# Optimization experiments

Hardware: AMD Instinct MI355X
Metric: run time of the kernel (lower is better)

Reference implementation:

```python
import jax, jax.numpy as jnp
import numpy as np
from jax import lax

G, K, KS = 4, 16, 3            # stripes, latents per stripe, support kernel
TEMP, TOPK_RATIO, GATE, EPS = 0.125, 0.125, 0.05, 1e-6


def _l2norm(v):
    # F.normalize(p=2, dim=-1): divide by max(norm, 1e-12)
    return v / jnp.maximum(jnp.linalg.norm(v, axis=-1, keepdims=True), 1e-12)


def _avg_pool3(x):
    # 3x3 avg pool, stride 1, pad 1, count_include_pad=True (torch default)
    s = lax.reduce_window(x, 0.0, lax.add, (1, 1, KS, KS), (1, 1, 1, 1),
                          [(0, 0), (0, 0), (KS // 2, KS // 2), (KS // 2, KS // 2)])
    return s / float(KS * KS)


def setup_inputs() -> dict:
    key = jax.random.key(0)
    k1, k2 = jax.random.split(key)
    x = jax.random.normal(k1, (64, 256, 64, 44), dtype=jnp.float32)
    latent_basis = jax.random.normal(k2, (G, K, 256), dtype=jnp.float32) * 0.05
    return {"x": x, "latent_basis": latent_basis}


def reference(x, latent_basis):
    n, c, h, w = x.shape
    hs = h // G
    # 'n c (g hs) w -> (n g) c hs w'
    sf = x.reshape(n, c, G, hs, w).transpose(0, 2, 1, 3, 4).reshape(n * G, c, hs, w)
    support_feat = _avg_pool3(sf)
    feat_flat = sf.reshape(n, G, c, hs * w).transpose(0, 1, 3, 2)          # n g p c
    supp_flat = support_feat.reshape(n, G, c, hs * w).transpose(0, 1, 3, 2)  # n g p c
    # active mask from detached energy
    e = jnp.mean(lax.stop_gradient(sf) ** 2, axis=1)                       # [n*G, hs, w]
    e = e / jnp.maximum(jnp.max(e, axis=(-2, -1), keepdims=True), EPS)
    am = (e > GATE).astype(jnp.float32)
    fb = (e > 0).astype(jnp.float32)
    use_fb = jnp.sum(am, axis=(-2, -1), keepdims=True) <= 0
    am = jnp.where(use_fb, fb, am).reshape(n, G, hs * w)                   # n g p
    # routing
    sfn = _l2norm(supp_flat)
    lb = _l2norm(latent_basis)                                             # g k c
    logits = jnp.einsum('ngpc,gkc->ngpk', sfn, lb) / TEMP
    route = jax.nn.softmax(logits, axis=-1)
    supp = route * am[..., None]                                           # n g p k
    pw = supp / jnp.maximum(jnp.sum(supp, axis=2, keepdims=True), EPS)
    tokens = jnp.einsum('ngpk,ngpc->ngkc', pw, feat_flat)                  # n g k c
    tokens = tokens.transpose(0, 3, 1, 2).reshape(n, c, G * K)             # n c (g k)
    # presence via top-k over positions
    p = supp.shape[2]
    topk = max(1, min(p, int(p * TOPK_RATIO)))
    vals = lax.top_k(supp.transpose(0, 1, 3, 2), topk)[0]                  # n g k topk
    pres = jnp.mean(vals, axis=-1).reshape(n, G * K)
    pres = pres / jnp.maximum(jnp.sum(pres, axis=1, keepdims=True), EPS)
    return tokens, pres
```

## Files before the change

### kernel.cpp

```cpp
#include <hip/hip_runtime.h>
#include <cstdint>


#define C_ 256
#define W_ 44
#define P_ 704
#define CH_STRIDE 2816
#define NB_STRIDE 720896
#define TOPK_ 88
#define GATE_ 0.05f
#define EPS_ 1e-6f

__global__ __launch_bounds__(256) void k_norm_basis(const float* __restrict__ lb,
                                                    float* __restrict__ lbn) {
  int gk = blockIdx.x;
  int t = threadIdx.x;
  float v = lb[gk * 256 + t];
  float ss = v * v;
  #pragma unroll
  for (int off = 32; off >= 1; off >>= 1) ss += __shfl_xor(ss, off);
  __shared__ float red[4];
  if ((t & 63) == 0) red[t >> 6] = ss;
  __syncthreads();
  float tot = red[0] + red[1] + red[2] + red[3];
  float scale = 1.f / fmaxf(sqrtf(tot), 1e-12f);
  int g = gk >> 4, k = gk & 15;
  lbn[((g * 256 + t) << 4) + k] = v * scale;
}

__global__ __launch_bounds__(1024) void k_route(const float* __restrict__ x,
                                                const float* __restrict__ lbn,
                                                float* __restrict__ supp_kp,
                                                float* __restrict__ supp_pk,
                                                float* __restrict__ invden_ws) {
  __shared__ float lbn_l[4096];
  __shared__ float rsl[11264];
  __shared__ float redA[16];
  __shared__ float redB[16];
  __shared__ float redM[2];
  __shared__ float red2[16 * 16];

  const int tid = threadIdx.x;
  const int w = tid >> 6;
  const int l = tid & 63;
  const bool act = (l < 44);
  const int s = blockIdx.x, n = s >> 2, g = s & 3;
  const int p = w * 44 + l;

  for (int i = tid; i < 4096; i += 1024) lbn_l[i] = lbn[(g << 12) + i];

  const int lsafe = act ? l : 0;
  const float* xb = x + (size_t)n * NB_STRIDE + (g * 16 + w) * 44 + lsafe;
  const float* xm = xb + ((w > 0)  ? -44 : 0);
  const float* xp = xb + ((w < 15) ?  44 : 0);
  const bool hm = (w > 0), hp = (w < 15);

  float rawdot[16];
  #pragma unroll
  for (int k = 0; k < 16; k++) rawdot[k] = 0.f;
  float sq = 0.f, pw2 = 0.f;

  __syncthreads();

  for (int c = 0; c < 256; c += 4) {
    float vm[4], v0[4], vp[4];
    #pragma unroll
    for (int j = 0; j < 4; j++) {
      const size_t o = (size_t)(c + j) * CH_STRIDE;
      vm[j] = xm[o]; v0[j] = xb[o]; vp[j] = xp[o];
    }
    #pragma unroll
    for (int j = 0; j < 4; j++) {
      float a  = act ? v0[j] : 0.f;
      float am_ = (act && hm) ? vm[j] : 0.f;
      float ap_ = (act && hp) ? vp[j] : 0.f;
      float vs = am_ + a + ap_;
      float lf = __shfl(vs, (l + 63) & 63);
      float rt = __shfl(vs, (l + 1) & 63);
      float win = lf + vs + rt;
      pw2 = fmaf(win, win, pw2);
      sq  = fmaf(a, a, sq);
      const float4* wp = (const float4*)&lbn_l[(c + j) << 4];
      float4 w0 = wp[0], w1 = wp[1], w2 = wp[2], w3 = wp[3];
      rawdot[0]  = fmaf(a, w0.x, rawdot[0]);  rawdot[1]  = fmaf(a, w0.y, rawdot[1]);
      rawdot[2]  = fmaf(a, w0.z, rawdot[2]);  rawdot[3]  = fmaf(a, w0.w, rawdot[3]);
      rawdot[4]  = fmaf(a, w1.x, rawdot[4]);  rawdot[5]  = fmaf(a, w1.y, rawdot[5]);
      rawdot[6]  = fmaf(a, w1.z, rawdot[6]);  rawdot[7]  = fmaf(a, w1.w, rawdot[7]);
      rawdot[8]  = fmaf(a, w2.x, rawdot[8]);  rawdot[9]  = fmaf(a, w2.y, rawdot[9]);
      rawdot[10] = fmaf(a, w2.z, rawdot[10]); rawdot[11] = fmaf(a, w2.w, rawdot[11]);
      rawdot[12] = fmaf(a, w3.x, rawdot[12]); rawdot[13] = fmaf(a, w3.y, rawdot[13]);
      rawdot[14] = fmaf(a, w3.z, rawdot[14]); rawdot[15] = fmaf(a, w3.w, rawdot[15]);
    }
  }

  float e_raw = sq * (1.f / 256.f);
  float m = e_raw;
  #pragma unroll
  for (int off = 32; off >= 1; off >>= 1) m = fmaxf(m, __shfl_xor(m, off));
  if (l == 0) redA[w] = m;
  __syncthreads();
  if (tid == 0) {
    float mm = redA[0];
    for (int w2 = 1; w2 < 16; w2++) mm = fmaxf(mm, redA[w2]);
    redM[0] = mm;
  }
  __syncthreads();
  float M = fmaxf(redM[0], EPS_);
  float e = e_raw / M;
  float am = (e > GATE_) ? 1.f : 0.f;
  float fb = (e_raw > 0.f) ? 1.f : 0.f;
  float a = am;
  #pragma unroll
  for (int off = 32; off >= 1; off >>= 1) a += __shfl_xor(a, off);
  if (l == 0) redB[w] = a;
  __syncthreads();
  if (tid == 0) {
    float sm = 0.f;
    for (int w2 = 0; w2 < 16; w2++) sm += redB[w2];
    redM[1] = sm;
  }
  __syncthreads();
  if (redM[1] <= 0.f) am = fb;

  if (act) {
    #pragma unroll
    for (int k = 0; k < 16; k++) rsl[k * 704 + p] = rawdot[k];
  }
  __syncthreads();

  float pd[16];
  #pragma unroll
  for (int k = 0; k < 16; k++) pd[k] = 0.f;
  if (act) {
    #pragma unroll
    for (int dy = -1; dy <= 1; dy++) {
      int yy = w + dy;
      if (yy < 0 || yy > 15) continue;
      #pragma unroll
      for (int dx = -1; dx <= 1; dx++) {
        int xx = l + dx;
        if (xx < 0 || xx > 43) continue;
        int pp = yy * 44 + xx;
        #pragma unroll
        for (int k = 0; k < 16; k++) pd[k] += rsl[k * 704 + pp];
      }
    }
  }

  float pnorm = sqrtf(pw2) * (1.f / 9.f);
  float invn = 1.f / fmaxf(pnorm, 1e-12f);
  float scl = invn * (8.f / 9.f);
  float li[16];
  float mx = -1e30f;
  #pragma unroll
  for (int k = 0; k < 16; k++) { li[k] = pd[k] * scl; mx = fmaxf(mx, li[k]); }
  float ssum = 0.f;
  #pragma unroll
  for (int k = 0; k < 16; k++) { li[k] = __expf(li[k] - mx); ssum += li[k]; }
  float rs2 = am / ssum;
  float supp[16];
  #pragma unroll
  for (int k = 0; k < 16; k++) supp[k] = li[k] * rs2;

  if (act) {
    float* sbp = supp_kp + (size_t)s * (16 * 704);
    #pragma unroll
    for (int k = 0; k < 16; k++) sbp[k * 704 + p] = supp[k];
    float* spk = supp_pk + ((size_t)s * 704 + p) * 16;
    #pragma unroll
    for (int kq = 0; kq < 4; kq++)
      ((float4*)spk)[kq] = make_float4(supp[kq*4+0], supp[kq*4+1],
                                       supp[kq*4+2], supp[kq*4+3]);
  }

  #pragma unroll
  for (int k = 0; k < 16; k++) {
    float v2 = act ? supp[k] : 0.f;
    #pragma unroll
    for (int off = 32; off >= 1; off >>= 1) v2 += __shfl_xor(v2, off);
    if (l == 0) red2[w * 16 + k] = v2;
  }
  __syncthreads();
  if (tid < 16) {
    float den = 0.f;
    for (int w2 = 0; w2 < 16; w2++) den += red2[w2 * 16 + tid];
    invden_ws[s * 16 + tid] = 1.f / fmaxf(den, EPS_);
  }
}

__global__ __launch_bounds__(256) void k_topk(const float* __restrict__ supp_kp,
                                              float* __restrict__ presraw) {
  const int blk = blockIdx.x;
  const int t = threadIdx.x;
  const int lane = t & 63, w = t >> 6;
  const float* v = supp_kp + (size_t)blk * 704;
  const bool h2 = (t < 192);
  uint32_t key0 = __float_as_uint(v[t]);
  uint32_t key1 = __float_as_uint(v[t + 256]);
  uint32_t key2 = h2 ? __float_as_uint(v[t + 512]) : 0u;

  __shared__ uint32_t hist[256];
  __shared__ uint32_t sarr[257];
  __shared__ uint32_t wsum[4];
  __shared__ uint32_t bc0, bc1;
  uint32_t prefix = 0, remaining = TOPK_;

  for (int b = 3; b >= 0; b--) {
    hist[t] = 0u;
    __syncthreads();
    const int shift = b * 8;
    uint32_t mhi = (b == 3) ? 0u : (0xFFFFFFFFu << (shift + 8));
    if ((key0 & mhi) == (prefix & mhi)) atomicAdd(&hist[(key0 >> shift) & 255u], 1u);
    if ((key1 & mhi) == (prefix & mhi)) atomicAdd(&hist[(key1 >> shift) & 255u], 1u);
    if (h2 && ((key2 & mhi) == (prefix & mhi))) atomicAdd(&hist[(key2 >> shift) & 255u], 1u);
    __syncthreads();

    uint32_t val = hist[t];
    #pragma unroll
    for (int off = 1; off < 64; off <<= 1) {
      uint32_t o = (uint32_t)__shfl_down((int)val, off);
      if (lane + off < 64) val += o;
    }
    if (lane == 0) wsum[w] = val;
    __syncthreads();
    uint32_t add = 0;
    for (int w2 = w + 1; w2 < 4; w2++) add += wsum[w2];
    sarr[t] = val + add;
    if (t == 0) sarr[256] = 0u;
    __syncthreads();
    uint32_t s_t = sarr[t], s_n = sarr[t + 1];
    if (s_t >= remaining && s_n < remaining) {
      bc0 = prefix | ((uint32_t)t << shift);
      bc1 = remaining - s_n;
    }
    __syncthreads();
    prefix = bc0; remaining = bc1;
    __syncthreads();
  }

  float tf = __uint_as_float(prefix);
  float sgt = 0.f;
  uint32_t cgt = 0;
  if (key0 > prefix) { sgt += __uint_as_float(key0); cgt++; }
  if (key1 > prefix) { sgt += __uint_as_float(key1); cgt++; }
  if (h2 && key2 > prefix) { sgt += __uint_as_float(key2); cgt++; }
  #pragma unroll
  for (int off = 32; off >= 1; off >>= 1) {
    sgt += __shfl_xor(sgt, off);
    cgt += __shfl_xor(cgt, off);
  }
  __shared__ float rsx[4];
  __shared__ uint32_t rcx[4];
  if (lane == 0) { rsx[w] = sgt; rcx[w] = cgt; }
  __syncthreads();
  if (t == 0) {
    float stot = rsx[0] + rsx[1] + rsx[2] + rsx[3];
    uint32_t ctot = rcx[0] + rcx[1] + rcx[2] + rcx[3];
    float top = stot + (float)(TOPK_ - ctot) * tf;
    presraw[blk] = top * (1.f / (float)TOPK_);
  }
}

__global__ __launch_bounds__(512, 4) void k_tokens(const float* __restrict__ x,
                                                   const float* __restrict__ supp_pk,
                                                   const float* __restrict__ invden,
                                                   float* __restrict__ out) {
  __shared__ float xl[4096];
  const int tid = threadIdx.x;
  const int bid = blockIdx.x;
  const int s = bid >> 1, chalf = bid & 1;
  const int n = s >> 2, g = s & 3;
  const int cl = tid & 127;
  const int q = tid >> 7;
  const int sblk = s * (704 * 16);

  const float* xs = x + (size_t)n * NB_STRIDE + (size_t)(chalf * 128) * CH_STRIDE + g * P_;

  const int li0 = tid, li1 = tid + 512;
  const int lc0 = li0 >> 3, lj0 = li0 & 7;
  const int lc1 = li1 >> 3, lj1 = li1 & 7;
  const float* gp0 = xs + (size_t)lc0 * CH_STRIDE + lj0 * 4;
  const float* gp1 = xs + (size_t)lc1 * CH_STRIDE + lj1 * 4;
  const int wo0 = lc0 * 32 + ((lj0 * 4) ^ ((lc0 & 7) * 4));
  const int wo1 = lc1 * 32 + ((lj1 * 4) ^ ((lc1 & 7) * 4));

  const int sw = (cl & 7) * 4;
  const int rbase = cl * 32;

  float acc[16];
  #pragma unroll
  for (int k = 0; k < 16; k++) acc[k] = 0.f;

  float4 r0 = *(const float4*)gp0;
  float4 r1 = *(const float4*)gp1;
  *(float4*)&xl[wo0] = r0;
  *(float4*)&xl[wo1] = r1;
  __syncthreads();

  for (int tt = 0; tt < 22; tt++) {
    const int p0 = tt * 32;
    float4 n0, n1;
    if (tt < 21) {
      n0 = *(const float4*)(gp0 + p0 + 32);
      n1 = *(const float4*)(gp1 + p0 + 32);
    }

    #pragma unroll
    for (int jj = 0; jj < 8; jj += 4) {
      const int pp0 = q * 8 + jj;
      float4 xv = *(const float4*)&xl[rbase + (pp0 ^ sw)];
      float xa[4] = {xv.x, xv.y, xv.z, xv.w};
      #pragma unroll
      for (int dj = 0; dj < 4; dj++) {
        int uofs = __builtin_amdgcn_readfirstlane(sblk + (p0 + pp0 + dj) * 16);
        const float4* sp = (const float4*)(supp_pk + uofs);
        float4 s0 = sp[0], s1 = sp[1], s2 = sp[2], s3 = sp[3];
        float a = xa[dj];
        acc[0]  += a * s0.x; acc[1]  += a * s0.y; acc[2]  += a * s0.z; acc[3]  += a * s0.w;
        acc[4]  += a * s1.x; acc[5]  += a * s1.y; acc[6]  += a * s1.z; acc[7]  += a * s1.w;
        acc[8]  += a * s2.x; acc[9]  += a * s2.y; acc[10] += a * s2.z; acc[11] += a * s2.w;
        acc[12] += a * s3.x; acc[13] += a * s3.y; acc[14] += a * s3.z; acc[15] += a * s3.w;
      }
    }

    __syncthreads();
    if (tt < 21) {
      *(float4*)&xl[wo0] = n0;
      *(float4*)&xl[wo1] = n1;
      __syncthreads();
    }
  }

  if (q >= 2) {
    float* dst = &xl[((q - 2) * 128 + cl) * 16];
    #pragma unroll
    for (int kq = 0; kq < 4; kq++)
      ((float4*)dst)[kq] = make_float4(acc[kq*4], acc[kq*4+1], acc[kq*4+2], acc[kq*4+3]);
  }
  __syncthreads();
  if (q < 2) {
    const float* src = &xl[(q * 128 + cl) * 16];
    #pragma unroll
    for (int k = 0; k < 16; k++) acc[k] += src[k];
  }
  __syncthreads();
  if (q == 1) {
    float* dst = &xl[cl * 16];
    #pragma unroll
    for (int kq = 0; kq < 4; kq++)
      ((float4*)dst)[kq] = make_float4(acc[kq*4], acc[kq*4+1], acc[kq*4+2], acc[kq*4+3]);
  }
  __syncthreads();
  if (q == 0) {
    const float* src = &xl[cl * 16];
    float* op = out + ((size_t)(n * 256 + chalf * 128 + cl) * 64) + g * 16;
    #pragma unroll
    for (int kq = 0; kq < 4; kq++) {
      int u = __builtin_amdgcn_readfirstlane(s * 16 + kq * 4);
      const float4 iv = *(const float4*)(invden + u);
      float4 o;
      o.x = (acc[kq*4+0] + src[kq*4+0]) * iv.x;
      o.y = (acc[kq*4+1] + src[kq*4+1]) * iv.y;
      o.z = (acc[kq*4+2] + src[kq*4+2]) * iv.z;
      o.w = (acc[kq*4+3] + src[kq*4+3]) * iv.w;
      ((float4*)op)[kq] = o;
    }
  }
}

__global__ __launch_bounds__(64) void k_pres(const float* __restrict__ presraw,
                                             float* __restrict__ out) {
  const int n = blockIdx.x, t = threadIdx.x;
  float v = presraw[n * 64 + t];
  float ssum = v;
  #pragma unroll
  for (int off = 32; off >= 1; off >>= 1) ssum += __shfl_xor(ssum, off);
  out[1048576 + n * 64 + t] = v / fmaxf(ssum, EPS_);
}

extern "C" void kernel_launch(void* const* d_in, const int* in_sizes, int n_in,
                              void* d_out, int out_size, void* d_ws, size_t ws_size,
                              hipStream_t stream) {
  (void)in_sizes; (void)n_in; (void)out_size; (void)ws_size;
  const float* x  = (const float*)d_in[0];
  const float* lb = (const float*)d_in[1];
  float* out = (float*)d_out;
  float* ws = (float*)d_ws;
  float* lbn_ws     = ws;
  float* invden_ws  = ws + 16384;
  float* presraw_ws = ws + 20480;
  float* supp_kp_ws = ws + 24576;
  float* supp_pk_ws = ws + 2908160;

  k_norm_basis<<<64, 256, 0, stream>>>(lb, lbn_ws);
  k_route<<<256, 1024, 0, stream>>>(x, lbn_ws, supp_kp_ws, supp_pk_ws, invden_ws);
  k_topk<<<4096, 256, 0, stream>>>(supp_kp_ws, presraw_ws);
  k_tokens<<<512, 512, 0, stream>>>(x, supp_pk_ws, invden_ws, out);
  k_pres<<<64, 64, 0, stream>>>(presraw_ws, out);
}
```

Before: 358.9 us.

## Split routing kernel over channel halves with partial-sum finalize kernel

The routing kernel previously ran one 1024-thread block per stripe (256 blocks), which leaves many compute units idle on a large GPU. It is now split into a partial kernel over two channel halves (512 blocks) that writes per-position dot products, energy and pooled-norm partials to workspace, plus a finalize kernel that sums them and runs the shared epilogue. This adds an extra launch and a round trip of the partials through global memory, and the old path is kept as a fallback when the workspace is too small. The tokens kernel's launch bounds are also raised to 8 blocks per CU, which may force fewer registers per thread.

```diff
diff --git a/kernel.cpp b/kernel.cpp
--- a/kernel.cpp
+++ b/kernel.cpp
@@ -10,6 +10,7 @@
 #define TOPK_ 88
 #define GATE_ 0.05f
 #define EPS_ 1e-6f
+#define PSLAB 12672
 
 __global__ __launch_bounds__(256) void k_norm_basis(const float* __restrict__ lb,
                                                     float* __restrict__ lbn) {
@@ -26,6 +27,109 @@
   float scale = 1.f / fmaxf(sqrtf(tot), 1e-12f);
   int g = gk >> 4, k = gk & 15;
   lbn[((g * 256 + t) << 4) + k] = v * scale;
+}
+
+__device__ __forceinline__ void route_epilogue(
+    int s, int w, int l, bool act, int p,
+    float* rawdot, float sq, float pw2,
+    float* rsl, float* redA, float* redB, float* redM, float* red2,
+    float* __restrict__ supp_kp, float* __restrict__ supp_pk,
+    float* __restrict__ invden_ws) {
+  const int tid = w * 64 + l;
+  float e_raw = sq * (1.f / 256.f);
+  float m = e_raw;
+  #pragma unroll
+  for (int off = 32; off >= 1; off >>= 1) m = fmaxf(m, __shfl_xor(m, off));
+  if (l == 0) redA[w] = m;
+  __syncthreads();
+  if (tid == 0) {
+    float mm = redA[0];
+    for (int w2 = 1; w2 < 16; w2++) mm = fmaxf(mm, redA[w2]);
+    redM[0] = mm;
+  }
+  __syncthreads();
+  float M = fmaxf(redM[0], EPS_);
+  float e = e_raw / M;
+  float am = (e > GATE_) ? 1.f : 0.f;
+  float fb = (e_raw > 0.f) ? 1.f : 0.f;
+  float a = am;
+  #pragma unroll
+  for (int off = 32; off >= 1; off >>= 1) a += __shfl_xor(a, off);
+  if (l == 0) redB[w] = a;
+  __syncthreads();
+  if (tid == 0) {
+    float sm = 0.f;
+    for (int w2 = 0; w2 < 16; w2++) sm += redB[w2];
+    redM[1] = sm;
+  }
+  __syncthreads();
+  if (redM[1] <= 0.f) am = fb;
+  __syncthreads();
+
+  if (act) {
+    #pragma unroll
+    for (int k = 0; k < 16; k++) rsl[k * 704 + p] = rawdot[k];
+  }
+  __syncthreads();
+
+  float pd[16];
+  #pragma unroll
+  for (int k = 0; k < 16; k++) pd[k] = 0.f;
+  if (act) {
+    #pragma unroll
+    for (int dy = -1; dy <= 1; dy++) {
+      int yy = w + dy;
+      if (yy < 0 || yy > 15) continue;
+      #pragma unroll
+      for (int dx = -1; dx <= 1; dx++) {
+        int xx = l + dx;
+        if (xx < 0 || xx > 43) continue;
+        int pp = yy * 44 + xx;
+        #pragma unroll
+        for (int k = 0; k < 16; k++) pd[k] += rsl[k * 704 + pp];
+      }
+    }
+  }
+
+  float pnorm = sqrtf(pw2) * (1.f / 9.f);
+  float invn = 1.f / fmaxf(pnorm, 1e-12f);
+  float scl = invn * (8.f / 9.f);
+  float li[16];
+  float mx = -1e30f;
+  #pragma unroll
+  for (int k = 0; k < 16; k++) { li[k] = pd[k] * scl; mx = fmaxf(mx, li[k]); }
+  float ssum = 0.f;
+  #pragma unroll
+  for (int k = 0; k < 16; k++) { li[k] = __expf(li[k] - mx); ssum += li[k]; }
+  float rs2 = am / ssum;
+  float supp[16];
+  #pragma unroll
+  for (int k = 0; k < 16; k++) supp[k] = li[k] * rs2;
+
+  if (act) {
+    float* sbp = supp_kp + (size_t)s * (16 * 704);
+    #pragma unroll
+    for (int k = 0; k < 16; k++) sbp[k * 704 + p] = supp[k];
+    float* spk = supp_pk + ((size_t)s * 704 + p) * 16;
+    #pragma unroll
+    for (int kq = 0; kq < 4; kq++)
+      ((float4*)spk)[kq] = make_float4(supp[kq*4+0], supp[kq*4+1],
+                                       supp[kq*4+2], supp[kq*4+3]);
+  }
+
+  #pragma unroll
+  for (int k = 0; k < 16; k++) {
+    float v2 = act ? supp[k] : 0.f;
+    #pragma unroll
+    for (int off = 32; off >= 1; off >>= 1) v2 += __shfl_xor(v2, off);
+    if (l == 0) red2[w * 16 + k] = v2;
+  }
+  __syncthreads();
+  if (tid < 16) {
+    float den = 0.f;
+    for (int w2 = 0; w2 < 16; w2++) den += red2[w2 * 16 + tid];
+    invden_ws[s * 16 + tid] = 1.f / fmaxf(den, EPS_);
+  }
 }
 
 __global__ __launch_bounds__(1024) void k_route(const float* __restrict__ x,
@@ -93,99 +197,109 @@
     }
   }
 
-  float e_raw = sq * (1.f / 256.f);
-  float m = e_raw;
-  #pragma unroll
-  for (int off = 32; off >= 1; off >>= 1) m = fmaxf(m, __shfl_xor(m, off));
-  if (l == 0) redA[w] = m;
-  __syncthreads();
-  if (tid == 0) {
-    float mm = redA[0];
-    for (int w2 = 1; w2 < 16; w2++) mm = fmaxf(mm, redA[w2]);
-    redM[0] = mm;
-  }
-  __syncthreads();
-  float M = fmaxf(redM[0], EPS_);
-  float e = e_raw / M;
-  float am = (e > GATE_) ? 1.f : 0.f;
-  float fb = (e_raw > 0.f) ? 1.f : 0.f;
-  float a = am;
-  #pragma unroll
-  for (int off = 32; off >= 1; off >>= 1) a += __shfl_xor(a, off);
-  if (l == 0) redB[w] = a;
-  __syncthreads();
-  if (tid == 0) {
-    float sm = 0.f;
-    for (int w2 = 0; w2 < 16; w2++) sm += redB[w2];
-    redM[1] = sm;
-  }
-  __syncthreads();
-  if (redM[1] <= 0.f) am = fb;
+  route_epilogue(s, w, l, act, p, rawdot, sq, pw2,
+                 rsl, redA, redB, redM, red2, supp_kp, supp_pk, invden_ws);
+}
+
+__global__ __launch_bounds__(1024) void k_route_part(const float* __restrict__ x,
+                                                     const float* __restrict__ lbn,
+                                                     float* __restrict__ part) {
+  __shared__ float lbn_l[2048];
+
+  const int tid = threadIdx.x;
+  const int w = tid >> 6;
+  const int l = tid & 63;
+  const bool act = (l < 44);
+  const int bid = blockIdx.x;
+  const int s = bid >> 1, h = bid & 1;
+  const int n = s >> 2, g = s & 3;
+  const int p = w * 44 + l;
+
+  for (int i = tid; i < 2048; i += 1024) lbn_l[i] = lbn[(g << 12) + (h << 11) + i];
+
+  const int lsafe = act ? l : 0;
+  const float* xb = x + (size_t)n * NB_STRIDE + (size_t)(h * 128) * CH_STRIDE
+                      + (g * 16 + w) * 44 + lsafe;
+  const float* xm = xb + ((w > 0)  ? -44 : 0);
+  const float* xp = xb + ((w < 15) ?  44 : 0);
+  const bool hm = (w > 0), hp = (w < 15);
+
+  float rawdot[16];
+  #pragma unroll
+  for (int k = 0; k < 16; k++) rawdot[k] = 0.f;
+  float sq = 0.f, pw2 = 0.f;
+
+  __syncthreads();
+
+  for (int c = 0; c < 128; c += 4) {
+    float vm[4], v0[4], vp[4];
+    #pragma unroll
+    for (int j = 0; j < 4; j++) {
+      const size_t o = (size_t)(c + j) * CH_STRIDE;
+      vm[j] = xm[o]; v0[j] = xb[o]; vp[j] = xp[o];
+    }
+    #pragma unroll
+    for (int j = 0; j < 4; j++) {
+      float a  = act ? v0[j] : 0.f;
+      float am_ = (act && hm) ? vm[j] : 0.f;
+      float ap_ = (act && hp) ? vp[j] : 0.f;
+      float vs = am_ + a + ap_;
+      float lf = __shfl(vs, (l + 63) & 63);
+      float rt = __shfl(vs, (l + 1) & 63);
+      float win = lf + vs + rt;
+      pw2 = fmaf(win, win, pw2);
+      sq  = fmaf(a, a, sq);
+      const float4* wp = (const float4*)&lbn_l[(c + j) << 4];
+      float4 w0 = wp[0], w1 = wp[1], w2 = wp[2], w3 = wp[3];
+      rawdot[0]  = fmaf(a, w0.x, rawdot[0]);  rawdot[1]  = fmaf(a, w0.y, rawdot[1]);
+      rawdot[2]  = fmaf(a, w0.z, rawdot[2]);  rawdot[3]  = fmaf(a, w0.w, rawdot[3]);
+      rawdot[4]  = fmaf(a, w1.x, rawdot[4]);  rawdot[5]  = fmaf(a, w1.y, rawdot[5]);
+      rawdot[6]  = fmaf(a, w1.z, rawdot[6]);  rawdot[7]  = fmaf(a, w1.w, rawdot[7]);
+      rawdot[8]  = fmaf(a, w2.x, rawdot[8]);  rawdot[9]  = fmaf(a, w2.y, rawdot[9]);
+      rawdot[10] = fmaf(a, w2.z, rawdot[10]); rawdot[11] = fmaf(a, w2.w, rawdot[11]);
+      rawdot[12] = fmaf(a, w3.x, rawdot[12]); rawdot[13] = fmaf(a, w3.y, rawdot[13]);
+      rawdot[14] = fmaf(a, w3.z, rawdot[14]); rawdot[15] = fmaf(a, w3.w, rawdot[15]);
+    }
+  }
 
   if (act) {
-    #pragma unroll
-    for (int k = 0; k < 16; k++) rsl[k * 704 + p] = rawdot[k];
-  }
-  __syncthreads();
-
-  float pd[16];
-  #pragma unroll
-  for (int k = 0; k < 16; k++) pd[k] = 0.f;
-  if (act) {
-    #pragma unroll
-    for (int dy = -1; dy <= 1; dy++) {
-      int yy = w + dy;
-      if (yy < 0 || yy > 15) continue;
-      #pragma unroll
-      for (int dx = -1; dx <= 1; dx++) {
-        int xx = l + dx;
-        if (xx < 0 || xx > 43) continue;
-        int pp = yy * 44 + xx;
-        #pragma unroll
-        for (int k = 0; k < 16; k++) pd[k] += rsl[k * 704 + pp];
-      }
-    }
-  }
-
-  float pnorm = sqrtf(pw2) * (1.f / 9.f);
-  float invn = 1.f / fmaxf(pnorm, 1e-12f);
-  float scl = invn * (8.f / 9.f);
-  float li[16];
-  float mx = -1e30f;
-  #pragma unroll
-  for (int k = 0; k < 16; k++) { li[k] = pd[k] * scl; mx = fmaxf(mx, li[k]); }
-  float ssum = 0.f;
-  #pragma unroll
-  for (int k = 0; k < 16; k++) { li[k] = __expf(li[k] - mx); ssum += li[k]; }
-  float rs2 = am / ssum;
-  float supp[16];
-  #pragma unroll
-  for (int k = 0; k < 16; k++) supp[k] = li[k] * rs2;
-
-  if (act) {
-    float* sbp = supp_kp + (size_t)s * (16 * 704);
-    #pragma unroll
-    for (int k = 0; k < 16; k++) sbp[k * 704 + p] = supp[k];
-    float* spk = supp_pk + ((size_t)s * 704 + p) * 16;
-    #pragma unroll
-    for (int kq = 0; kq < 4; kq++)
-      ((float4*)spk)[kq] = make_float4(supp[kq*4+0], supp[kq*4+1],
-                                       supp[kq*4+2], supp[kq*4+3]);
-  }
-
-  #pragma unroll
-  for (int k = 0; k < 16; k++) {
-    float v2 = act ? supp[k] : 0.f;
-    #pragma unroll
-    for (int off = 32; off >= 1; off >>= 1) v2 += __shfl_xor(v2, off);
-    if (l == 0) red2[w * 16 + k] = v2;
-  }
-  __syncthreads();
-  if (tid < 16) {
-    float den = 0.f;
-    for (int w2 = 0; w2 < 16; w2++) den += red2[w2 * 16 + tid];
-    invden_ws[s * 16 + tid] = 1.f / fmaxf(den, EPS_);
-  }
+    float* pb = part + (size_t)bid * PSLAB;
+    #pragma unroll
+    for (int k = 0; k < 16; k++) pb[k * 704 + p] = rawdot[k];
+    pb[16 * 704 + p] = sq;
+    pb[17 * 704 + p] = pw2;
+  }
+}
+
+__global__ __launch_bounds__(1024) void k_route_fin(const float* __restrict__ part,
+                                                    float* __restrict__ supp_kp,
+                                                    float* __restrict__ supp_pk,
+                                                    float* __restrict__ invden_ws) {
+  __shared__ float rsl[11264];
+  __shared__ float redA[16];
+  __shared__ float redB[16];
+  __shared__ float redM[2];
+  __shared__ float red2[16 * 16];
+
+  const int tid = threadIdx.x;
+  const int w = tid >> 6;
+  const int l = tid & 63;
+  const bool act = (l < 44);
+  const int s = blockIdx.x;
+  const int p = w * 44 + l;
+  const int psafe = act ? p : w * 44;
+
+  const float* pa = part + (size_t)(s * 2 + 0) * PSLAB;
+  const float* pb = part + (size_t)(s * 2 + 1) * PSLAB;
+
+  float rawdot[16];
+  #pragma unroll
+  for (int k = 0; k < 16; k++) rawdot[k] = pa[k * 704 + psafe] + pb[k * 704 + psafe];
+  float sq  = act ? (pa[16 * 704 + psafe] + pb[16 * 704 + psafe]) : 0.f;
+  float pw2 = act ? (pa[17 * 704 + psafe] + pb[17 * 704 + psafe]) : 0.f;
+
+  route_epilogue(s, w, l, act, p, rawdot, sq, pw2,
+                 rsl, redA, redB, redM, red2, supp_kp, supp_pk, invden_ws);
 }
 
 __global__ __launch_bounds__(256) void k_topk(const float* __restrict__ supp_kp,
@@ -261,7 +375,7 @@
   }
 }
 
-__global__ __launch_bounds__(512, 4) void k_tokens(const float* __restrict__ x,
+__global__ __launch_bounds__(512, 8) void k_tokens(const float* __restrict__ x,
                                                    const float* __restrict__ supp_pk,
                                                    const float* __restrict__ invden,
                                                    float* __restrict__ out) {
@@ -381,7 +495,7 @@
 extern "C" void kernel_launch(void* const* d_in, const int* in_sizes, int n_in,
                               void* d_out, int out_size, void* d_ws, size_t ws_size,
                               hipStream_t stream) {
-  (void)in_sizes; (void)n_in; (void)out_size; (void)ws_size;
+  (void)in_sizes; (void)n_in; (void)out_size;
   const float* x  = (const float*)d_in[0];
   const float* lb = (const float*)d_in[1];
   float* out = (float*)d_out;
@@ -391,9 +505,17 @@
   float* presraw_ws = ws + 20480;
   float* supp_kp_ws = ws + 24576;
   float* supp_pk_ws = ws + 2908160;
+  float* part_ws    = ws + 5791744;
+
+  const bool split_ok = ws_size >= (size_t)12279808 * sizeof(float);
 
   k_norm_basis<<<64, 256, 0, stream>>>(lb, lbn_ws);
-  k_route<<<256, 1024, 0, stream>>>(x, lbn_ws, supp_kp_ws, supp_pk_ws, invden_ws);
+  if (split_ok) {
+    k_route_part<<<512, 1024, 0, stream>>>(x, lbn_ws, part_ws);
+    k_route_fin<<<256, 1024, 0, stream>>>(part_ws, supp_kp_ws, supp_pk_ws, invden_ws);
+  } else {
+    k_route<<<256, 1024, 0, stream>>>(x, lbn_ws, supp_kp_ws, supp_pk_ws, invden_ws);
+  }
   k_topk<<<4096, 256, 0, stream>>>(supp_kp_ws, presraw_ws);
   k_tokens<<<512, 512, 0, stream>>>(x, supp_pk_ws, invden_ws, out);
   k_pres<<<64, 64, 0, stream>>>(presraw_ws, out);
```

Result: no change. 365.6 us (+1.9%).
